# Optimization experiments

Hardware: AMD Instinct MI355X
Metric: run time of the kernel (lower is better)

The kernel has to match this reference:

```python
import jax, jax.numpy as jnp
import numpy as np

B, T, E = 4, 2048, 768
H = 12
D = E // H  # head dim = 64


def setup_inputs() -> dict:
    key = jax.random.key(0)
    ks = jax.random.split(key, 9)
    s = 0.02
    x = jax.random.normal(ks[0], (B, T, E), dtype=jnp.float32)
    Wq = jax.random.normal(ks[1], (E, E), dtype=jnp.float32) * s
    bq = jnp.zeros((E,), dtype=jnp.float32)
    Wk = jax.random.normal(ks[2], (E, E), dtype=jnp.float32) * s
    bk = jnp.zeros((E,), dtype=jnp.float32)
    Wv = jax.random.normal(ks[3], (E, E), dtype=jnp.float32) * s
    bv = jnp.zeros((E,), dtype=jnp.float32)
    Wo = jax.random.normal(ks[4], (E, E), dtype=jnp.float32) * s
    bo = jnp.zeros((E,), dtype=jnp.float32)
    # causal mask, broadcastable [1,1,T,T]; masked_fill where mask == 0
    attn_mask = jnp.tril(jnp.ones((T, T), dtype=jnp.int32))[None, None, :, :]
    return {"x": x, "Wq": Wq, "bq": bq, "Wk": Wk, "bk": bk,
            "Wv": Wv, "bv": bv, "Wo": Wo, "bo": bo, "attn_mask": attn_mask}


def reference(x, Wq, bq, Wk, bk, Wv, bv, Wo, bo, attn_mask):
    # QKV projections: [B,T,E] -> [B,T,E]
    q = x @ Wq + bq
    k = x @ Wk + bk
    v = x @ Wv + bv
    # split heads -> [B,H,T,D]
    def split(t):
        return t.reshape(B, T, H, D).transpose(0, 2, 1, 3)
    q, k, v = split(q), split(k), split(v)
    # eager attention: full [B,H,T,T] scores (faithful to the torch module)
    att = jnp.einsum('bhqd,bhkd->bhqk', q, k) * (1.0 / np.sqrt(D).astype(np.float32))
    att = jnp.where(attn_mask == 0, jnp.float32(-jnp.inf), att)
    att_weights = jax.nn.softmax(att, axis=-1)
    # attn_dropout rate = 0.0 (eval) -> identity
    y = jnp.einsum('bhqk,bhkd->bhqd', att_weights, v)
    y = y.transpose(0, 2, 1, 3).reshape(B, T, E)
    y = y @ Wo + bo  # proj_dropout rate = 0.0 -> identity
    return (y, att_weights)
```

## Files before the change

### kernel.cpp

```cpp
#include <hip/hip_runtime.h>
#include <hip/hip_bf16.h>
#include <stdint.h>

#define BB 4
#define HH 12
#define TT 2048
#define DD 64
#define EE 768
#define BT (BB*TT)
#define NQKV (3*EE)

typedef __attribute__((ext_vector_type(8))) short bf16x8;
typedef __attribute__((ext_vector_type(4))) float f32x4;

__device__ __forceinline__ unsigned short f2bf(float f){
  union { float f; unsigned int u; } x; x.f = f;
  unsigned int u = x.u;
  unsigned int r = (u + 0x7fffu + ((u >> 16) & 1u)) >> 16;
  return (unsigned short)r;
}

__global__ void cvt_bf16(const float* __restrict__ src, unsigned short* __restrict__ dst, int n){
  int i = (blockIdx.x*blockDim.x + threadIdx.x)*4;
  if (i < n){
    float4 v = *(const float4*)&src[i];
    ushort4 o;
    o.x = f2bf(v.x); o.y = f2bf(v.y); o.z = f2bf(v.z); o.w = f2bf(v.w);
    *(ushort4*)&dst[i] = o;
  }
}

__global__ void transpose_cvt_768(const float* __restrict__ src,
                                  unsigned short* __restrict__ dst){
  __shared__ float tile[32][33];
  int bx = blockIdx.x*32, by = blockIdx.y*32;
  int tx = threadIdx.x, ty = threadIdx.y;
  #pragma unroll
  for (int i=0;i<32;i+=8) tile[ty+i][tx] = src[(size_t)(by+ty+i)*EE + bx+tx];
  __syncthreads();
  #pragma unroll
  for (int i=0;i<32;i+=8) dst[(size_t)(bx+ty+i)*EE + by+tx] = f2bf(tile[tx][ty+i]);
}

__device__ __forceinline__ void gemm_core_128(
    const unsigned short* __restrict__ A, const unsigned short* __restrict__ Bt,
    int K, int mBase, int nBase,
    unsigned short* Alds, unsigned short* Blds,
    f32x4 acc[4][4])
{
  const int tid = threadIdx.x;
  const int lane = tid & 63, wave = tid >> 6;
  const int wm = wave & 1, wn = wave >> 1;
  const int ln15 = lane & 15, quad = lane >> 4;
  #pragma unroll
  for (int mt=0; mt<4; ++mt)
    #pragma unroll
    for (int nt=0; nt<4; ++nt)
      acc[mt][nt] = (f32x4){0.f,0.f,0.f,0.f};

  for (int k0=0; k0<K; k0+=32){
    #pragma unroll
    for (int i=0;i<2;i++){
      int idx = tid + i*256;
      int r = idx >> 2, seg = idx & 3;
      *(uint4*)&Alds[r*40 + seg*8] = *(const uint4*)&A[(size_t)(mBase + r)*K + k0 + seg*8];
      *(uint4*)&Blds[r*40 + seg*8] = *(const uint4*)&Bt[(size_t)(nBase + r)*K + k0 + seg*8];
    }
    __syncthreads();
    bf16x8 af[4], bfr[4];
    #pragma unroll
    for (int mt=0;mt<4;++mt) af[mt]  = *(const bf16x8*)&Alds[(wm*64 + mt*16 + ln15)*40 + quad*8];
    #pragma unroll
    for (int nt=0;nt<4;++nt) bfr[nt] = *(const bf16x8*)&Blds[(wn*64 + nt*16 + ln15)*40 + quad*8];
    #pragma unroll
    for (int mt=0;mt<4;++mt)
      #pragma unroll
      for (int nt=0;nt<4;++nt)
        acc[mt][nt] = __builtin_amdgcn_mfma_f32_16x16x32_bf16(af[mt], bfr[nt], acc[mt][nt], 0,0,0);
    __syncthreads();
  }
}

#define QSCALE 0.18033688f
__global__ __launch_bounds__(256,2) void gemm_qkv(
    const unsigned short* __restrict__ x, const unsigned short* __restrict__ WtQKV,
    const float* __restrict__ bq, const float* __restrict__ bk,
    const float* __restrict__ bv,
    unsigned short* __restrict__ q_ws, unsigned short* __restrict__ k_ws,
    unsigned short* __restrict__ v_ws)
{
  __shared__ unsigned short Alds[128*40];
  __shared__ unsigned short Blds[128*40];
  const int mBase = blockIdx.y*128, nBase = blockIdx.x*128;
  f32x4 acc[4][4];
  gemm_core_128(x, WtQKV, EE, mBase, nBase, Alds, Blds, acc);

  const int tid = threadIdx.x, lane = tid&63, wave = tid>>6;
  const int wm = wave&1, wn = wave>>1, ln15 = lane&15, quad = lane>>4;
  const int which = nBase / EE;
  const float* bias = (which==0) ? bq : ((which==1) ? bk : bv);
  const float sc = (which==0) ? QSCALE : 1.0f;
  #pragma unroll
  for (int nt=0;nt<4;++nt){
    int col = nBase + wn*64 + nt*16 + ln15;
    int n0 = col - which*EE;
    int h = n0 >> 6, d = n0 & 63;
    float bsv = bias[n0];
    #pragma unroll
    for (int mt=0;mt<4;++mt){
      #pragma unroll
      for (int reg=0;reg<4;++reg){
        int row = mBase + wm*64 + mt*16 + quad*4 + reg;
        int b = row >> 11, t = row & 2047;
        unsigned short o = f2bf((acc[mt][nt][reg] + bsv)*sc);
        if (which==0)      q_ws[((size_t)(b*HH + h)*TT + t)*DD + d] = o;
        else if (which==1) k_ws[((size_t)(b*HH + h)*TT + t)*DD + d] = o;
        else               v_ws[((size_t)(b*HH + h)*DD + d)*TT + t] = o;
      }
    }
  }
}

__global__ __launch_bounds__(256,2) void gemm_proj(
    const unsigned short* __restrict__ yin, const unsigned short* __restrict__ WoT,
    const float* __restrict__ bo, float* __restrict__ out)
{
  __shared__ unsigned short Alds[128*40];
  __shared__ unsigned short Blds[128*40];
  const int mBase = blockIdx.y*128, nBase = blockIdx.x*128;
  f32x4 acc[4][4];
  gemm_core_128(yin, WoT, EE, mBase, nBase, Alds, Blds, acc);

  const int tid = threadIdx.x, lane = tid&63, wave = tid>>6;
  const int wm = wave&1, wn = wave>>1, ln15 = lane&15, quad = lane>>4;
  #pragma unroll
  for (int nt=0;nt<4;++nt){
    int col = nBase + wn*64 + nt*16 + ln15;
    float bsv = bo[col];
    #pragma unroll
    for (int mt=0;mt<4;++mt){
      #pragma unroll
      for (int reg=0;reg<4;++reg){
        int row = mBase + wm*64 + mt*16 + quad*4 + reg;
        out[(size_t)row*EE + col] = acc[mt][nt][reg] + bsv;
      }
    }
  }
}

__global__ __launch_bounds__(256,4) void attn_kernel(
    const unsigned short* __restrict__ q_ws, const unsigned short* __restrict__ k_ws,
    const unsigned short* __restrict__ v_ws, float* __restrict__ att,
    unsigned short* __restrict__ y_ws)
{
  const int sid = blockIdx.x;
  const int qt  = 31 - ((sid >> 3) & 31);
  const int bh  = (sid & 7) + ((sid >> 8) << 3);
  const int b  = bh / HH, h = bh - b*HH;
  const int tid = threadIdx.x, lane = tid&63, wave = tid>>6;
  const int quad = lane>>4, ln15 = lane&15;

  __shared__ unsigned short Ks[2][64*72];
  __shared__ unsigned short Vts[64*72];
  __shared__ unsigned short Ps[4*16*72];

  const unsigned short* Qg = q_ws + ((size_t)bh*TT + qt*64)*DD;
  const unsigned short* Kg = k_ws + (size_t)bh*TT*DD;
  const unsigned short* Vg = v_ws + (size_t)bh*DD*TT;
  float* attb = att + ((size_t)bh*TT + (size_t)qt*64)*TT;

  const int seg  = tid & 7;
  const int rowA = tid >> 3;
  const int rowB = rowA + 32;

  uint4 ka0 = *(const uint4*)&Kg[(size_t)rowA*DD + seg*8];
  uint4 ka1 = *(const uint4*)&Kg[(size_t)rowB*DD + seg*8];

  bf16x8 aq0 = *(const bf16x8*)&Qg[(size_t)(wave*16+ln15)*DD + quad*8];
  bf16x8 aq1 = *(const bf16x8*)&Qg[(size_t)(wave*16+ln15)*DD + 32 + quad*8];

  const float NEG = -30000.0f;
  const int qrow0 = qt*64 + wave*16 + quad*4;

  float lp[4] = {0.f,0.f,0.f,0.f};
  for (int kt=0; kt<=qt; ++kt){
    unsigned short* Kb = Ks[kt&1];
    *(uint4*)&Kb[rowA*72 + seg*8] = ka0;
    *(uint4*)&Kb[rowB*72 + seg*8] = ka1;
    __syncthreads();
    if (kt < qt){
      ka0 = *(const uint4*)&Kg[(size_t)((kt+1)*64+rowA)*DD + seg*8];
      ka1 = *(const uint4*)&Kg[(size_t)((kt+1)*64+rowB)*DD + seg*8];
    }
    f32x4 s[4];
    #pragma unroll
    for (int nt=0;nt<4;++nt){
      s[nt] = (f32x4){0.f,0.f,0.f,0.f};
      bf16x8 bk0 = *(const bf16x8*)&Kb[(nt*16+ln15)*72 + quad*8];
      bf16x8 bk1 = *(const bf16x8*)&Kb[(nt*16+ln15)*72 + 32 + quad*8];
      s[nt] = __builtin_amdgcn_mfma_f32_16x16x32_bf16(aq0, bk0, s[nt], 0,0,0);
      s[nt] = __builtin_amdgcn_mfma_f32_16x16x32_bf16(aq1, bk1, s[nt], 0,0,0);
    }
    const bool diag = (kt==qt);
    #pragma unroll
    for (int reg=0;reg<4;++reg){
      #pragma unroll
      for (int nt=0;nt<4;++nt){
        float v = s[nt][reg];
        if (diag && (kt*64 + nt*16 + ln15) > qrow0+reg) v = NEG;
        lp[reg] += exp2f(v);
      }
    }
  }
  float rl[4];
  #pragma unroll
  for (int r=0;r<4;++r){
    float ss = lp[r];
    ss += __shfl_xor(ss, 1);
    ss += __shfl_xor(ss, 2);
    ss += __shfl_xor(ss, 4);
    ss += __shfl_xor(ss, 8);
    rl[r] = 1.f / ss;
  }

  f32x4 yacc[4];
  #pragma unroll
  for (int nt=0;nt<4;++nt) yacc[nt] = (f32x4){0.f,0.f,0.f,0.f};

  uint4 kb0 = *(const uint4*)&Kg[(size_t)rowA*DD + seg*8];
  uint4 kb1 = *(const uint4*)&Kg[(size_t)rowB*DD + seg*8];
  uint4 vb0 = *(const uint4*)&Vg[(size_t)rowA*TT + seg*8];
  uint4 vb1 = *(const uint4*)&Vg[(size_t)rowB*TT + seg*8];
  __syncthreads();

  for (int kt=0; kt<=qt; ++kt){
    unsigned short* Kb = Ks[kt&1];
    *(uint4*)&Kb[rowA*72 + seg*8]  = kb0;
    *(uint4*)&Kb[rowB*72 + seg*8]  = kb1;
    *(uint4*)&Vts[rowA*72 + seg*8] = vb0;
    *(uint4*)&Vts[rowB*72 + seg*8] = vb1;
    __syncthreads();
    if (kt < qt){
      kb0 = *(const uint4*)&Kg[(size_t)((kt+1)*64+rowA)*DD + seg*8];
      kb1 = *(const uint4*)&Kg[(size_t)((kt+1)*64+rowB)*DD + seg*8];
      vb0 = *(const uint4*)&Vg[(size_t)rowA*TT + (kt+1)*64 + seg*8];
      vb1 = *(const uint4*)&Vg[(size_t)rowB*TT + (kt+1)*64 + seg*8];
    }
    f32x4 s[4];
    #pragma unroll
    for (int nt=0;nt<4;++nt){
      s[nt] = (f32x4){0.f,0.f,0.f,0.f};
      bf16x8 bk0 = *(const bf16x8*)&Kb[(nt*16+ln15)*72 + quad*8];
      bf16x8 bk1 = *(const bf16x8*)&Kb[(nt*16+ln15)*72 + 32 + quad*8];
      s[nt] = __builtin_amdgcn_mfma_f32_16x16x32_bf16(aq0, bk0, s[nt], 0,0,0);
      s[nt] = __builtin_amdgcn_mfma_f32_16x16x32_bf16(aq1, bk1, s[nt], 0,0,0);
    }
    const bool diag = (kt==qt);
    #pragma unroll
    for (int nt=0;nt<4;++nt){
      int key = kt*64 + nt*16 + ln15;
      #pragma unroll
      for (int reg=0;reg<4;++reg){
        float v = s[nt][reg];
        if (diag && key > qrow0+reg) v = NEG;
        float p = exp2f(v)*rl[reg];
        attb[(size_t)(wave*16 + quad*4 + reg)*TT + key] = p;
        Ps[wave*1152 + (quad*4+reg)*72 + nt*16 + ln15] = f2bf(p);
      }
    }
    bf16x8 ap0 = *(const bf16x8*)&Ps[(wave*16+ln15)*72 + quad*8];
    bf16x8 ap1 = *(const bf16x8*)&Ps[(wave*16+ln15)*72 + 32 + quad*8];
    #pragma unroll
    for (int nt=0;nt<4;++nt){
      bf16x8 bv0 = *(const bf16x8*)&Vts[(nt*16+ln15)*72 + quad*8];
      bf16x8 bv1 = *(const bf16x8*)&Vts[(nt*16+ln15)*72 + 32 + quad*8];
      yacc[nt] = __builtin_amdgcn_mfma_f32_16x16x32_bf16(ap0, bv0, yacc[nt], 0,0,0);
      yacc[nt] = __builtin_amdgcn_mfma_f32_16x16x32_bf16(ap1, bv1, yacc[nt], 0,0,0);
    }
    __syncthreads();
  }

  {
    int wstart = (qt+1)*64;
    int r = tid>>2;
    float4 z = make_float4(0.f,0.f,0.f,0.f);
    for (int c = wstart + (tid&3)*4; c < TT; c += 16)
      *(float4*)&attb[(size_t)r*TT + c] = z;
  }

  #pragma unroll
  for (int nt=0;nt<4;++nt){
    #pragma unroll
    for (int reg=0;reg<4;++reg){
      int t = qt*64 + wave*16 + quad*4 + reg;
      size_t row = (size_t)b*TT + t;
      int col = h*DD + nt*16 + ln15;
      y_ws[row*EE + col] = f2bf(yacc[nt][reg]);
    }
  }
}

extern "C" void kernel_launch(void* const* d_in, const int* in_sizes, int n_in,
                              void* d_out, int out_size, void* d_ws, size_t ws_size,
                              hipStream_t stream){
  (void)in_sizes; (void)n_in; (void)out_size; (void)ws_size;
  const float* x  = (const float*)d_in[0];
  const float* Wq = (const float*)d_in[1];
  const float* bq = (const float*)d_in[2];
  const float* Wk = (const float*)d_in[3];
  const float* bk = (const float*)d_in[4];
  const float* Wv = (const float*)d_in[5];
  const float* bv = (const float*)d_in[6];
  const float* Wo = (const float*)d_in[7];
  const float* bo = (const float*)d_in[8];

  float* out = (float*)d_out;
  float* y_out   = out;
  float* att_out = out + (size_t)BT*EE;

  unsigned short* ws = (unsigned short*)d_ws;
  unsigned short* x_bf   = ws;
  unsigned short* WtQKV  = x_bf  + (size_t)BT*EE;
  unsigned short* WoT    = WtQKV + (size_t)NQKV*EE;
  unsigned short* q_ws   = WoT   + (size_t)EE*EE;
  unsigned short* k_ws   = q_ws  + (size_t)BB*HH*TT*DD;
  unsigned short* v_ws   = k_ws  + (size_t)BB*HH*TT*DD;
  unsigned short* y_ws   = v_ws  + (size_t)BB*HH*TT*DD;

  cvt_bf16<<<(BT*EE)/(256*4), 256, 0, stream>>>(x, x_bf, BT*EE);
  dim3 tb(32,8), tg(24,24);
  transpose_cvt_768<<<tg, tb, 0, stream>>>(Wq, WtQKV);
  transpose_cvt_768<<<tg, tb, 0, stream>>>(Wk, WtQKV + (size_t)EE*EE);
  transpose_cvt_768<<<tg, tb, 0, stream>>>(Wv, WtQKV + (size_t)2*EE*EE);
  transpose_cvt_768<<<tg, tb, 0, stream>>>(Wo, WoT);

  gemm_qkv<<<dim3(NQKV/128, BT/128), 256, 0, stream>>>(x_bf, WtQKV, bq, bk, bv, q_ws, k_ws, v_ws);
  attn_kernel<<<dim3(32*BB*HH), 256, 0, stream>>>(q_ws, k_ws, v_ws, att_out, y_ws);
  gemm_proj<<<dim3(EE/128, BT/128), 256, 0, stream>>>(y_ws, WoT, bo, y_out);
}
```

Before: 1.126 ms.

## Split attention into row-sum and emit kernels, double-buffer V, merge weight transposes

Splits the attention kernel in two. The first kernel computes softmax row sums and stores their reciprocals in a workspace. The second recomputes the scores and writes the attention probabilities and the output, using double-buffered K and V in shared memory so one barrier per iteration can be dropped. The four weight-transpose launches are also merged into a single 3D-grid launch. In exchange, the kernels run sequentially with an extra launch and global round trip for the row sums, and the emit kernel uses more shared memory with a lower occupancy hint (3 instead of 4 blocks).

```diff
diff --git a/kernel.cpp b/kernel.cpp
--- a/kernel.cpp
+++ b/kernel.cpp
@@ -30,9 +30,14 @@
   }
 }
 
-__global__ void transpose_cvt_768(const float* __restrict__ src,
-                                  unsigned short* __restrict__ dst){
+__global__ void transpose_cvt_all(const float* __restrict__ Wq, const float* __restrict__ Wk,
+                                  const float* __restrict__ Wv, const float* __restrict__ Wo,
+                                  unsigned short* __restrict__ WtQKV,
+                                  unsigned short* __restrict__ WoT){
   __shared__ float tile[32][33];
+  const int z = blockIdx.z;
+  const float* src = (z==0) ? Wq : (z==1) ? Wk : (z==2) ? Wv : Wo;
+  unsigned short* dst = (z<3) ? (WtQKV + (size_t)z*EE*EE) : WoT;
   int bx = blockIdx.x*32, by = blockIdx.y*32;
   int tx = threadIdx.x, ty = threadIdx.y;
   #pragma unroll
@@ -148,26 +153,20 @@
   }
 }
 
-__global__ __launch_bounds__(256,4) void attn_kernel(
+__global__ __launch_bounds__(256,4) void attn_lsum(
     const unsigned short* __restrict__ q_ws, const unsigned short* __restrict__ k_ws,
-    const unsigned short* __restrict__ v_ws, float* __restrict__ att,
-    unsigned short* __restrict__ y_ws)
+    float* __restrict__ rl_ws)
 {
   const int sid = blockIdx.x;
   const int qt  = 31 - ((sid >> 3) & 31);
   const int bh  = (sid & 7) + ((sid >> 8) << 3);
-  const int b  = bh / HH, h = bh - b*HH;
   const int tid = threadIdx.x, lane = tid&63, wave = tid>>6;
   const int quad = lane>>4, ln15 = lane&15;
 
   __shared__ unsigned short Ks[2][64*72];
-  __shared__ unsigned short Vts[64*72];
-  __shared__ unsigned short Ps[4*16*72];
 
   const unsigned short* Qg = q_ws + ((size_t)bh*TT + qt*64)*DD;
   const unsigned short* Kg = k_ws + (size_t)bh*TT*DD;
-  const unsigned short* Vg = v_ws + (size_t)bh*DD*TT;
-  float* attb = att + ((size_t)bh*TT + (size_t)qt*64)*TT;
 
   const int seg  = tid & 7;
   const int rowA = tid >> 3;
@@ -212,7 +211,7 @@
       }
     }
   }
-  float rl[4];
+  float4 rlv;
   #pragma unroll
   for (int r=0;r<4;++r){
     float ss = lp[r];
@@ -220,25 +219,61 @@
     ss += __shfl_xor(ss, 2);
     ss += __shfl_xor(ss, 4);
     ss += __shfl_xor(ss, 8);
-    rl[r] = 1.f / ss;
-  }
-
-  f32x4 yacc[4];
-  #pragma unroll
-  for (int nt=0;nt<4;++nt) yacc[nt] = (f32x4){0.f,0.f,0.f,0.f};
+    ((float*)&rlv)[r] = 1.f / ss;
+  }
+  if (ln15 == 0)
+    *(float4*)&rl_ws[(size_t)bh*TT + qt*64 + wave*16 + quad*4] = rlv;
+}
+
+__global__ __launch_bounds__(256,3) void attn_emit(
+    const unsigned short* __restrict__ q_ws, const unsigned short* __restrict__ k_ws,
+    const unsigned short* __restrict__ v_ws, const float* __restrict__ rl_ws,
+    float* __restrict__ att, unsigned short* __restrict__ y_ws)
+{
+  const int sid = blockIdx.x;
+  const int qt  = 31 - ((sid >> 3) & 31);
+  const int bh  = (sid & 7) + ((sid >> 8) << 3);
+  const int b  = bh / HH, h = bh - b*HH;
+  const int tid = threadIdx.x, lane = tid&63, wave = tid>>6;
+  const int quad = lane>>4, ln15 = lane&15;
+
+  __shared__ unsigned short Ks[2][64*72];
+  __shared__ unsigned short Vts[2][64*72];
+  __shared__ unsigned short Ps[4*16*72];
+
+  const unsigned short* Qg = q_ws + ((size_t)bh*TT + qt*64)*DD;
+  const unsigned short* Kg = k_ws + (size_t)bh*TT*DD;
+  const unsigned short* Vg = v_ws + (size_t)bh*DD*TT;
+  float* attb = att + ((size_t)bh*TT + (size_t)qt*64)*TT;
+
+  const int seg  = tid & 7;
+  const int rowA = tid >> 3;
+  const int rowB = rowA + 32;
 
   uint4 kb0 = *(const uint4*)&Kg[(size_t)rowA*DD + seg*8];
   uint4 kb1 = *(const uint4*)&Kg[(size_t)rowB*DD + seg*8];
   uint4 vb0 = *(const uint4*)&Vg[(size_t)rowA*TT + seg*8];
   uint4 vb1 = *(const uint4*)&Vg[(size_t)rowB*TT + seg*8];
-  __syncthreads();
+
+  bf16x8 aq0 = *(const bf16x8*)&Qg[(size_t)(wave*16+ln15)*DD + quad*8];
+  bf16x8 aq1 = *(const bf16x8*)&Qg[(size_t)(wave*16+ln15)*DD + 32 + quad*8];
+  float4 rlv = *(const float4*)&rl_ws[(size_t)bh*TT + qt*64 + wave*16 + quad*4];
+  const float rl[4] = {rlv.x, rlv.y, rlv.z, rlv.w};
+
+  const float NEG = -30000.0f;
+  const int qrow0 = qt*64 + wave*16 + quad*4;
+
+  f32x4 yacc[4];
+  #pragma unroll
+  for (int nt=0;nt<4;++nt) yacc[nt] = (f32x4){0.f,0.f,0.f,0.f};
 
   for (int kt=0; kt<=qt; ++kt){
     unsigned short* Kb = Ks[kt&1];
-    *(uint4*)&Kb[rowA*72 + seg*8]  = kb0;
-    *(uint4*)&Kb[rowB*72 + seg*8]  = kb1;
-    *(uint4*)&Vts[rowA*72 + seg*8] = vb0;
-    *(uint4*)&Vts[rowB*72 + seg*8] = vb1;
+    unsigned short* Vb = Vts[kt&1];
+    *(uint4*)&Kb[rowA*72 + seg*8] = kb0;
+    *(uint4*)&Kb[rowB*72 + seg*8] = kb1;
+    *(uint4*)&Vb[rowA*72 + seg*8] = vb0;
+    *(uint4*)&Vb[rowB*72 + seg*8] = vb1;
     __syncthreads();
     if (kt < qt){
       kb0 = *(const uint4*)&Kg[(size_t)((kt+1)*64+rowA)*DD + seg*8];
@@ -272,12 +307,11 @@
     bf16x8 ap1 = *(const bf16x8*)&Ps[(wave*16+ln15)*72 + 32 + quad*8];
     #pragma unroll
     for (int nt=0;nt<4;++nt){
-      bf16x8 bv0 = *(const bf16x8*)&Vts[(nt*16+ln15)*72 + quad*8];
-      bf16x8 bv1 = *(const bf16x8*)&Vts[(nt*16+ln15)*72 + 32 + quad*8];
+      bf16x8 bv0 = *(const bf16x8*)&Vb[(nt*16+ln15)*72 + quad*8];
+      bf16x8 bv1 = *(const bf16x8*)&Vb[(nt*16+ln15)*72 + 32 + quad*8];
       yacc[nt] = __builtin_amdgcn_mfma_f32_16x16x32_bf16(ap0, bv0, yacc[nt], 0,0,0);
       yacc[nt] = __builtin_amdgcn_mfma_f32_16x16x32_bf16(ap1, bv1, yacc[nt], 0,0,0);
     }
-    __syncthreads();
   }
 
   {
@@ -326,15 +360,13 @@
   unsigned short* k_ws   = q_ws  + (size_t)BB*HH*TT*DD;
   unsigned short* v_ws   = k_ws  + (size_t)BB*HH*TT*DD;
   unsigned short* y_ws   = v_ws  + (size_t)BB*HH*TT*DD;
+  float*          rl_ws  = (float*)(y_ws + (size_t)BT*EE);
 
   cvt_bf16<<<(BT*EE)/(256*4), 256, 0, stream>>>(x, x_bf, BT*EE);
-  dim3 tb(32,8), tg(24,24);
-  transpose_cvt_768<<<tg, tb, 0, stream>>>(Wq, WtQKV);
-  transpose_cvt_768<<<tg, tb, 0, stream>>>(Wk, WtQKV + (size_t)EE*EE);
-  transpose_cvt_768<<<tg, tb, 0, stream>>>(Wv, WtQKV + (size_t)2*EE*EE);
-  transpose_cvt_768<<<tg, tb, 0, stream>>>(Wo, WoT);
+  transpose_cvt_all<<<dim3(24,24,4), dim3(32,8), 0, stream>>>(Wq, Wk, Wv, Wo, WtQKV, WoT);
 
   gemm_qkv<<<dim3(NQKV/128, BT/128), 256, 0, stream>>>(x_bf, WtQKV, bq, bk, bv, q_ws, k_ws, v_ws);
-  attn_kernel<<<dim3(32*BB*HH), 256, 0, stream>>>(q_ws, k_ws, v_ws, att_out, y_ws);
+  attn_lsum<<<dim3(32*BB*HH), 256, 0, stream>>>(q_ws, k_ws, rl_ws);
+  attn_emit<<<dim3(32*BB*HH), 256, 0, stream>>>(q_ws, k_ws, v_ws, rl_ws, att_out, y_ws);
   gemm_proj<<<dim3(EE/128, BT/128), 256, 0, stream>>>(y_ws, WoT, bo, y_out);
 }
```

New measurement: 1.158 ms. 2.8% more time.

## Double-buffer V tiles, peel diagonal tile, merge weight transposes into one launch

Applied to the files above, without the earlier changes.

The attention kernel now double-buffers the V tile in shared memory, which lets it drop the trailing barrier per iteration. It also peels the causal-diagonal tile out of both loops so the steady-state loops carry no mask or bounds branches, and precomputes per-row pointers into the attention output. The four weight transpose launches are merged into one 3D-grid launch to cut launch overhead. The extra LDS for the second V buffer led to lowering launch bounds from 4 to 3 blocks per CU, which may reduce occupancy.

```diff
diff --git a/kernel.cpp b/kernel.cpp
--- a/kernel.cpp
+++ b/kernel.cpp
@@ -30,9 +30,14 @@
   }
 }
 
-__global__ void transpose_cvt_768(const float* __restrict__ src,
-                                  unsigned short* __restrict__ dst){
+__global__ void transpose_cvt_all(const float* __restrict__ Wq, const float* __restrict__ Wk,
+                                  const float* __restrict__ Wv, const float* __restrict__ Wo,
+                                  unsigned short* __restrict__ WtQKV,
+                                  unsigned short* __restrict__ WoT){
   __shared__ float tile[32][33];
+  const int z = blockIdx.z;
+  const float* src = (z==0) ? Wq : (z==1) ? Wk : (z==2) ? Wv : Wo;
+  unsigned short* dst = (z<3) ? (WtQKV + (size_t)z*EE*EE) : WoT;
   int bx = blockIdx.x*32, by = blockIdx.y*32;
   int tx = threadIdx.x, ty = threadIdx.y;
   #pragma unroll
@@ -148,7 +153,7 @@
   }
 }
 
-__global__ __launch_bounds__(256,4) void attn_kernel(
+__global__ __launch_bounds__(256,3) void attn_kernel(
     const unsigned short* __restrict__ q_ws, const unsigned short* __restrict__ k_ws,
     const unsigned short* __restrict__ v_ws, float* __restrict__ att,
     unsigned short* __restrict__ y_ws)
@@ -161,7 +166,7 @@
   const int quad = lane>>4, ln15 = lane&15;
 
   __shared__ unsigned short Ks[2][64*72];
-  __shared__ unsigned short Vts[64*72];
+  __shared__ unsigned short Vts[2][64*72];
   __shared__ unsigned short Ps[4*16*72];
 
   const unsigned short* Qg = q_ws + ((size_t)bh*TT + qt*64)*DD;
@@ -180,18 +185,16 @@
   bf16x8 aq1 = *(const bf16x8*)&Qg[(size_t)(wave*16+ln15)*DD + 32 + quad*8];
 
   const float NEG = -30000.0f;
-  const int qrow0 = qt*64 + wave*16 + quad*4;
+  const int qloc = wave*16 + quad*4;
 
   float lp[4] = {0.f,0.f,0.f,0.f};
-  for (int kt=0; kt<=qt; ++kt){
+  for (int kt=0; kt<qt; ++kt){
     unsigned short* Kb = Ks[kt&1];
     *(uint4*)&Kb[rowA*72 + seg*8] = ka0;
     *(uint4*)&Kb[rowB*72 + seg*8] = ka1;
     __syncthreads();
-    if (kt < qt){
-      ka0 = *(const uint4*)&Kg[(size_t)((kt+1)*64+rowA)*DD + seg*8];
-      ka1 = *(const uint4*)&Kg[(size_t)((kt+1)*64+rowB)*DD + seg*8];
-    }
+    ka0 = *(const uint4*)&Kg[(size_t)((kt+1)*64+rowA)*DD + seg*8];
+    ka1 = *(const uint4*)&Kg[(size_t)((kt+1)*64+rowB)*DD + seg*8];
     f32x4 s[4];
     #pragma unroll
     for (int nt=0;nt<4;++nt){
@@ -201,16 +204,34 @@
       s[nt] = __builtin_amdgcn_mfma_f32_16x16x32_bf16(aq0, bk0, s[nt], 0,0,0);
       s[nt] = __builtin_amdgcn_mfma_f32_16x16x32_bf16(aq1, bk1, s[nt], 0,0,0);
     }
-    const bool diag = (kt==qt);
-    #pragma unroll
-    for (int reg=0;reg<4;++reg){
+    #pragma unroll
+    for (int reg=0;reg<4;++reg)
+      #pragma unroll
+      for (int nt=0;nt<4;++nt)
+        lp[reg] += exp2f(s[nt][reg]);
+  }
+  {
+    unsigned short* Kb = Ks[qt&1];
+    *(uint4*)&Kb[rowA*72 + seg*8] = ka0;
+    *(uint4*)&Kb[rowB*72 + seg*8] = ka1;
+    __syncthreads();
+    f32x4 s[4];
+    #pragma unroll
+    for (int nt=0;nt<4;++nt){
+      s[nt] = (f32x4){0.f,0.f,0.f,0.f};
+      bf16x8 bk0 = *(const bf16x8*)&Kb[(nt*16+ln15)*72 + quad*8];
+      bf16x8 bk1 = *(const bf16x8*)&Kb[(nt*16+ln15)*72 + 32 + quad*8];
+      s[nt] = __builtin_amdgcn_mfma_f32_16x16x32_bf16(aq0, bk0, s[nt], 0,0,0);
+      s[nt] = __builtin_amdgcn_mfma_f32_16x16x32_bf16(aq1, bk1, s[nt], 0,0,0);
+    }
+    #pragma unroll
+    for (int reg=0;reg<4;++reg)
       #pragma unroll
       for (int nt=0;nt<4;++nt){
         float v = s[nt][reg];
-        if (diag && (kt*64 + nt*16 + ln15) > qrow0+reg) v = NEG;
+        if ((nt*16+ln15) > qloc+reg) v = NEG;
         lp[reg] += exp2f(v);
       }
-    }
   }
   float rl[4];
   #pragma unroll
@@ -233,19 +254,22 @@
   uint4 vb1 = *(const uint4*)&Vg[(size_t)rowB*TT + seg*8];
   __syncthreads();
 
-  for (int kt=0; kt<=qt; ++kt){
+  float* attrow[4];
+  #pragma unroll
+  for (int reg=0;reg<4;++reg) attrow[reg] = attb + (size_t)(qloc+reg)*TT;
+
+  for (int kt=0; kt<qt; ++kt){
     unsigned short* Kb = Ks[kt&1];
-    *(uint4*)&Kb[rowA*72 + seg*8]  = kb0;
-    *(uint4*)&Kb[rowB*72 + seg*8]  = kb1;
-    *(uint4*)&Vts[rowA*72 + seg*8] = vb0;
-    *(uint4*)&Vts[rowB*72 + seg*8] = vb1;
-    __syncthreads();
-    if (kt < qt){
-      kb0 = *(const uint4*)&Kg[(size_t)((kt+1)*64+rowA)*DD + seg*8];
-      kb1 = *(const uint4*)&Kg[(size_t)((kt+1)*64+rowB)*DD + seg*8];
-      vb0 = *(const uint4*)&Vg[(size_t)rowA*TT + (kt+1)*64 + seg*8];
-      vb1 = *(const uint4*)&Vg[(size_t)rowB*TT + (kt+1)*64 + seg*8];
-    }
+    unsigned short* Vb = Vts[kt&1];
+    *(uint4*)&Kb[rowA*72 + seg*8] = kb0;
+    *(uint4*)&Kb[rowB*72 + seg*8] = kb1;
+    *(uint4*)&Vb[rowA*72 + seg*8] = vb0;
+    *(uint4*)&Vb[rowB*72 + seg*8] = vb1;
+    __syncthreads();
+    kb0 = *(const uint4*)&Kg[(size_t)((kt+1)*64+rowA)*DD + seg*8];
+    kb1 = *(const uint4*)&Kg[(size_t)((kt+1)*64+rowB)*DD + seg*8];
+    vb0 = *(const uint4*)&Vg[(size_t)rowA*TT + (kt+1)*64 + seg*8];
+    vb1 = *(const uint4*)&Vg[(size_t)rowB*TT + (kt+1)*64 + seg*8];
     f32x4 s[4];
     #pragma unroll
     for (int nt=0;nt<4;++nt){
@@ -255,16 +279,52 @@
       s[nt] = __builtin_amdgcn_mfma_f32_16x16x32_bf16(aq0, bk0, s[nt], 0,0,0);
       s[nt] = __builtin_amdgcn_mfma_f32_16x16x32_bf16(aq1, bk1, s[nt], 0,0,0);
     }
-    const bool diag = (kt==qt);
     #pragma unroll
     for (int nt=0;nt<4;++nt){
       int key = kt*64 + nt*16 + ln15;
+      #pragma unroll
+      for (int reg=0;reg<4;++reg){
+        float p = exp2f(s[nt][reg])*rl[reg];
+        attrow[reg][key] = p;
+        Ps[wave*1152 + (quad*4+reg)*72 + nt*16 + ln15] = f2bf(p);
+      }
+    }
+    bf16x8 ap0 = *(const bf16x8*)&Ps[(wave*16+ln15)*72 + quad*8];
+    bf16x8 ap1 = *(const bf16x8*)&Ps[(wave*16+ln15)*72 + 32 + quad*8];
+    #pragma unroll
+    for (int nt=0;nt<4;++nt){
+      bf16x8 bv0 = *(const bf16x8*)&Vb[(nt*16+ln15)*72 + quad*8];
+      bf16x8 bv1 = *(const bf16x8*)&Vb[(nt*16+ln15)*72 + 32 + quad*8];
+      yacc[nt] = __builtin_amdgcn_mfma_f32_16x16x32_bf16(ap0, bv0, yacc[nt], 0,0,0);
+      yacc[nt] = __builtin_amdgcn_mfma_f32_16x16x32_bf16(ap1, bv1, yacc[nt], 0,0,0);
+    }
+  }
+  {
+    unsigned short* Kb = Ks[qt&1];
+    unsigned short* Vb = Vts[qt&1];
+    *(uint4*)&Kb[rowA*72 + seg*8] = kb0;
+    *(uint4*)&Kb[rowB*72 + seg*8] = kb1;
+    *(uint4*)&Vb[rowA*72 + seg*8] = vb0;
+    *(uint4*)&Vb[rowB*72 + seg*8] = vb1;
+    __syncthreads();
+    f32x4 s[4];
+    #pragma unroll
+    for (int nt=0;nt<4;++nt){
+      s[nt] = (f32x4){0.f,0.f,0.f,0.f};
+      bf16x8 bk0 = *(const bf16x8*)&Kb[(nt*16+ln15)*72 + quad*8];
+      bf16x8 bk1 = *(const bf16x8*)&Kb[(nt*16+ln15)*72 + 32 + quad*8];
+      s[nt] = __builtin_amdgcn_mfma_f32_16x16x32_bf16(aq0, bk0, s[nt], 0,0,0);
+      s[nt] = __builtin_amdgcn_mfma_f32_16x16x32_bf16(aq1, bk1, s[nt], 0,0,0);
+    }
+    #pragma unroll
+    for (int nt=0;nt<4;++nt){
+      int key = qt*64 + nt*16 + ln15;
       #pragma unroll
       for (int reg=0;reg<4;++reg){
         float v = s[nt][reg];
-        if (diag && key > qrow0+reg) v = NEG;
+        if ((nt*16+ln15) > qloc+reg) v = NEG;
         float p = exp2f(v)*rl[reg];
-        attb[(size_t)(wave*16 + quad*4 + reg)*TT + key] = p;
+        attrow[reg][key] = p;
         Ps[wave*1152 + (quad*4+reg)*72 + nt*16 + ln15] = f2bf(p);
       }
     }
@@ -272,12 +332,11 @@
     bf16x8 ap1 = *(const bf16x8*)&Ps[(wave*16+ln15)*72 + 32 + quad*8];
     #pragma unroll
     for (int nt=0;nt<4;++nt){
-      bf16x8 bv0 = *(const bf16x8*)&Vts[(nt*16+ln15)*72 + quad*8];
-      bf16x8 bv1 = *(const bf16x8*)&Vts[(nt*16+ln15)*72 + 32 + quad*8];
+      bf16x8 bv0 = *(const bf16x8*)&Vb[(nt*16+ln15)*72 + quad*8];
+      bf16x8 bv1 = *(const bf16x8*)&Vb[(nt*16+ln15)*72 + 32 + quad*8];
       yacc[nt] = __builtin_amdgcn_mfma_f32_16x16x32_bf16(ap0, bv0, yacc[nt], 0,0,0);
       yacc[nt] = __builtin_amdgcn_mfma_f32_16x16x32_bf16(ap1, bv1, yacc[nt], 0,0,0);
     }
-    __syncthreads();
   }
 
   {
@@ -292,7 +351,7 @@
   for (int nt=0;nt<4;++nt){
     #pragma unroll
     for (int reg=0;reg<4;++reg){
-      int t = qt*64 + wave*16 + quad*4 + reg;
+      int t = qt*64 + qloc + reg;
       size_t row = (size_t)b*TT + t;
       int col = h*DD + nt*16 + ln15;
       y_ws[row*EE + col] = f2bf(yacc[nt][reg]);
@@ -328,11 +387,7 @@
   unsigned short* y_ws   = v_ws  + (size_t)BB*HH*TT*DD;
 
   cvt_bf16<<<(BT*EE)/(256*4), 256, 0, stream>>>(x, x_bf, BT*EE);
-  dim3 tb(32,8), tg(24,24);
-  transpose_cvt_768<<<tg, tb, 0, stream>>>(Wq, WtQKV);
-  transpose_cvt_768<<<tg, tb, 0, stream>>>(Wk, WtQKV + (size_t)EE*EE);
-  transpose_cvt_768<<<tg, tb, 0, stream>>>(Wv, WtQKV + (size_t)2*EE*EE);
-  transpose_cvt_768<<<tg, tb, 0, stream>>>(Wo, WoT);
+  transpose_cvt_all<<<dim3(24,24,4), dim3(32,8), 0, stream>>>(Wq, Wk, Wv, Wo, WtQKV, WoT);
 
   gemm_qkv<<<dim3(NQKV/128, BT/128), 256, 0, stream>>>(x_bf, WtQKV, bq, bk, bv, q_ws, k_ws, v_ws);
   attn_kernel<<<dim3(32*BB*HH), 256, 0, stream>>>(q_ws, k_ws, v_ws, att_out, y_ws);
```

Measured after the change: 1.140 ms. No clear change (+1.2%).
